# Optimization experiments

Measured on AMD Instinct MI355X. Metric: run time of the kernel, lower is better.

Reference implementation:

```python
import jax, jax.numpy as jnp
import numpy as np

IN_C, HID_C, OUT_C = 256, 512, 256
B, N = 8, 4096


def setup_inputs() -> dict:
    key = jax.random.key(0)
    ks = jax.random.split(key, 6)
    x = jax.random.normal(ks[0], (B, N, IN_C), dtype=jnp.float32)
    A = jax.random.uniform(ks[1], (B, N, N), dtype=jnp.float32)
    # Glorot-ish init for the two GCN layer weights + zero biases (PyG default bias=True)
    W1 = jax.random.normal(ks[2], (IN_C, HID_C), dtype=jnp.float32) * (1.0 / np.sqrt(IN_C))
    b1 = jnp.zeros((HID_C,), dtype=jnp.float32)
    W2 = jax.random.normal(ks[3], (HID_C, OUT_C), dtype=jnp.float32) * (1.0 / np.sqrt(HID_C))
    b2 = jnp.zeros((OUT_C,), dtype=jnp.float32)
    return {"x": x, "A": A, "W1": W1, "b1": b1, "W2": W2, "b2": b2}


def _gcn_norm(A):
    # dense equivalent of PyG gcn_norm with add_self_loops: A_hat = A + I,
    # norm = D^{-1/2} A_hat D^{-1/2}, with deg==0 -> 0 (inf guarded)
    A_hat = A + jnp.eye(A.shape[-1], dtype=A.dtype)  # [B,N,N]
    deg = A_hat.sum(axis=-1)                          # [B,N]
    d_inv_sqrt = jnp.where(deg > 0, jax.lax.rsqrt(jnp.maximum(deg, 1e-12)), 0.0)
    return d_inv_sqrt[:, :, None] * A_hat * d_inv_sqrt[:, None, :]


def reference(x, A, W1, b1, W2, b2):
    nrm = _gcn_norm(A)  # [B,N,N]
    # layer 1: out = A_hat_norm @ (x W1) + b1, then ReLU (dropout is identity in eval)
    h = jax.nn.relu(jnp.einsum('bij,bjh->bih', nrm, x @ W1) + b1)
    # layer 2
    out = jnp.einsum('bij,bjo->bio', nrm, h @ W2) + b2
    return out
```

## Files before the change

### kernel.cpp

```cpp
#include <hip/hip_runtime.h>
#include <stdint.h>

#define NN    4096
#define BATCH 8
#define IC    256
#define HC    512
#define OC    256
#define MTOT  (BATCH * NN)

typedef float    f32x4  __attribute__((ext_vector_type(4)));
typedef __bf16   bf16x8 __attribute__((ext_vector_type(8)));
typedef uint16_t u16x8  __attribute__((ext_vector_type(8)));
typedef uint16_t u16x4  __attribute__((ext_vector_type(4)));

__device__ __forceinline__ uint16_t f2b(float f) {
  union { float f; uint32_t u; } v; v.f = f;
  return (uint16_t)((v.u + 0x7FFFu + ((v.u >> 16) & 1u)) >> 16);
}

__device__ __forceinline__ void gl_lds16(const void* g, void* l) {
  __builtin_amdgcn_global_load_lds(
      (const __attribute__((address_space(1))) uint32_t*)g,
      (__attribute__((address_space(3))) uint32_t*)l, 16, 0, 0);
}

__global__ __launch_bounds__(512) void prep_kernel(const float* __restrict__ A,
                                                   uint16_t* __restrict__ Abf,
                                                   float* __restrict__ dinv) {
  const int bid = blockIdx.x;
  const int b = bid & 7, mt = bid >> 3;
  const int t = threadIdx.x;
  const int r = t >> 2, g = t & 3;
  const int rowl = mt * 128 + r;
  const float* Ap = A + ((size_t)b * NN + rowl) * NN + g * 8;
  uint16_t* Op = Abf + ((size_t)(b * 32 + mt) << 19) + r * 32 + ((g ^ (r & 3)) << 3);
  float s = 0.f;
  for (int kt = 0; kt < 128; ++kt) {
    f32x4 a0 = *(const f32x4*)(Ap + kt * 32);
    f32x4 a1 = *(const f32x4*)(Ap + kt * 32 + 4);
    int dj = rowl - (kt * 32 + g * 8);
    u16x8 o;
#pragma unroll
    for (int e = 0; e < 4; ++e) {
      float v0 = a0[e], v1 = a1[e];
      s += v0 + v1;
      if (dj == e)     v0 += 1.f;
      if (dj == e + 4) v1 += 1.f;
      o[e] = f2b(v0); o[e + 4] = f2b(v1);
    }
    *(u16x8*)(Op + (size_t)kt * 4096) = o;
  }
  __shared__ float red[512];
  red[t] = s;
  __syncthreads();
  if (t < 128) {
    float deg = red[t * 4] + red[t * 4 + 1] + red[t * 4 + 2] + red[t * 4 + 3] + 1.0f;
    dinv[b * NN + mt * 128 + t] = 1.0f / sqrtf(deg);
  }
}

template<bool ABF16, int KTOT, int NC>
__global__ __launch_bounds__(256, 2) void xw_kernel(const void* __restrict__ Av,
                                                    const float* __restrict__ W,
                                                    const float* __restrict__ dinv,
                                                    uint16_t* __restrict__ Vt) {
  constexpr int LDT = 72;
  __shared__ uint16_t smem[18432];
  uint16_t* as_ = smem;
  uint16_t* wt_ = smem + 9216;
  const int t = threadIdx.x;
  const int m0 = blockIdx.x * 128;
  const int n0 = blockIdx.y * 128;
  const int lane = t & 63, wid = t >> 6;
  const int wm = wid >> 1, wn = wid & 1;
  f32x4 acc[4][4] = {};

  for (int kt = 0; kt < KTOT / 64; ++kt) {
    const int k0 = kt * 64;
    __syncthreads();
    if constexpr (!ABF16) {
      const float* Ap = (const float*)Av;
      const int c4 = t & 15, r0 = t >> 4;
#pragma unroll
      for (int i = 0; i < 8; ++i) {
        int r = r0 + 16 * i;
        f32x4 v = *(const f32x4*)(Ap + (size_t)(m0 + r) * KTOT + k0 + c4 * 4);
        uint32_t lo = f2b(v[0]) | ((uint32_t)f2b(v[1]) << 16);
        uint32_t hi = f2b(v[2]) | ((uint32_t)f2b(v[3]) << 16);
        *(uint2*)&as_[r * LDT + c4 * 4] = make_uint2(lo, hi);
      }
    } else {
      const uint16_t* Ap = (const uint16_t*)Av;
      const int c8 = t & 7, r0 = t >> 3;
#pragma unroll
      for (int i = 0; i < 4; ++i) {
        int r = r0 + 32 * i;
        u16x8 v = *(const u16x8*)(Ap + (size_t)(m0 + r) * KTOT + k0 + c8 * 8);
        *(u16x8*)&as_[r * LDT + c8 * 8] = v;
      }
    }
    {
      const int n4 = t & 31, kq = t >> 5;
#pragma unroll
      for (int i = 0; i < 8; ++i) {
        int k = kq + 8 * i;
        f32x4 v = *(const f32x4*)(W + (size_t)(k0 + k) * NC + n0 + n4 * 4);
        uint16_t hv[4] = { f2b(v[0]), f2b(v[1]), f2b(v[2]), f2b(v[3]) };
#pragma unroll
        for (int w = 0; w < 4; ++w) {
          int we = (w + n4) & 3;
          wt_[(n4 * 4 + we) * LDT + k] = hv[we];
        }
      }
    }
    __syncthreads();
#pragma unroll
    for (int kk = 0; kk < 2; ++kk) {
      bf16x8 bfr[4], afr[4];
#pragma unroll
      for (int fn = 0; fn < 4; ++fn)
        bfr[fn] = *(const bf16x8*)&wt_[(wn * 64 + fn * 16 + (lane & 15)) * LDT + kk * 32 + (lane >> 4) * 8];
#pragma unroll
      for (int fm = 0; fm < 4; ++fm)
        afr[fm] = *(const bf16x8*)&as_[(wm * 64 + fm * 16 + (lane & 15)) * LDT + kk * 32 + (lane >> 4) * 8];
#pragma unroll
      for (int fm = 0; fm < 4; ++fm)
#pragma unroll
        for (int fn = 0; fn < 4; ++fn)
          acc[fm][fn] = __builtin_amdgcn_mfma_f32_16x16x32_bf16(afr[fm], bfr[fn], acc[fm][fn], 0, 0, 0);
    }
  }
  const int b = m0 >> 12;
  const int klocal = m0 & 4095;
  __syncthreads();
  uint16_t* lv = smem;
#pragma unroll
  for (int fm = 0; fm < 4; ++fm)
#pragma unroll
    for (int fn = 0; fn < 4; ++fn) {
      int nloc = wn * 64 + fn * 16 + (lane & 15);
      int ml0  = wm * 64 + fm * 16 + (lane >> 4) * 4;
      u16x4 pk;
#pragma unroll
      for (int r = 0; r < 4; ++r)
        pk[r] = f2b(acc[fm][fn][r] * dinv[m0 + ml0 + r]);
      *(u16x4*)&lv[nloc * 144 + ml0] = pk;
    }
  __syncthreads();
#pragma unroll
  for (int i = 0; i < 8; ++i) {
    int nloc = (t >> 4) + 16 * i;
    int ch = t & 15;
    u16x8 v = *(const u16x8*)&lv[nloc * 144 + ch * 8];
    int nglob = n0 + nloc;
    int ktv = (klocal >> 5) + (ch >> 2);
    int s = (ch & 3) ^ (nglob & 3);
    *(u16x8*)(Vt + (((size_t)b * 128 + ktv) * NC + nglob) * 32 + s * 8) = v;
  }
}

template<int NC_, bool RELU>
__global__ __launch_bounds__(512, 2) void agg_kernel(const uint16_t* __restrict__ Abf,
                                                     const uint16_t* __restrict__ Vt,
                                                     const float* __restrict__ dinv,
                                                     const float* __restrict__ bias,
                                                     uint16_t* __restrict__ Hout,
                                                     float* __restrict__ Fout) {
  constexpr int FN  = NC_ / 64;
  constexpr int WNE = NC_ / 4;
  constexpr int VPW = NC_ / 128;
  __shared__ uint16_t as_[2][4096];
  __shared__ uint16_t vt_[2][NC_ * 32];

  const int t = threadIdx.x;
  const int lane = t & 63, wid = t >> 6;
  const int wm = wid >> 2, wn = wid & 3;
  const int fr = lane & 15, c = lane >> 4;
  const int bid = blockIdx.x;
  const int b = bid & 7, mt = bid >> 3;

  const uint16_t* Abase = Abf + ((size_t)(b * 32 + mt) << 19);
  const uint16_t* Vbase = Vt + (size_t)b * NC_ * 4096;

  auto stage = [&](int kt, int buf) {
    const uint16_t* At = Abase + (size_t)kt * 4096;
    const uint16_t* Vtile = Vbase + (size_t)kt * (NC_ * 32);
    gl_lds16(At + wid * 512 + lane * 8, &as_[buf][wid * 512]);
#pragma unroll
    for (int i = 0; i < VPW; ++i) {
      int cv = wid * VPW + i;
      gl_lds16(Vtile + cv * 512 + lane * 8, &vt_[buf][cv * 512]);
    }
  };

  f32x4 acc[4][FN] = {};

  stage(0, 0);
  asm volatile("s_waitcnt vmcnt(0)" ::: "memory");
  asm volatile("" ::: "memory");
  __builtin_amdgcn_s_barrier();
  __builtin_amdgcn_sched_barrier(0);

  for (int kt = 0; kt < 128; ++kt) {
    const int cur = kt & 1;
    if (kt < 127) stage(kt + 1, cur ^ 1);
    bf16x8 afr[4], bfr[FN];
#pragma unroll
    for (int fm = 0; fm < 4; ++fm) {
      int row = wm * 64 + fm * 16 + fr;
      afr[fm] = *(const bf16x8*)&as_[cur][row * 32 + ((c ^ (row & 3)) << 3)];
    }
#pragma unroll
    for (int fn = 0; fn < FN; ++fn) {
      int n = wn * WNE + fn * 16 + fr;
      bfr[fn] = *(const bf16x8*)&vt_[cur][n * 32 + ((c ^ (n & 3)) << 3)];
    }
    __builtin_amdgcn_s_setprio(1);
#pragma unroll
    for (int fm = 0; fm < 4; ++fm)
#pragma unroll
      for (int fn = 0; fn < FN; ++fn)
        acc[fm][fn] = __builtin_amdgcn_mfma_f32_16x16x32_bf16(afr[fm], bfr[fn], acc[fm][fn], 0, 0, 0);
    __builtin_amdgcn_s_setprio(0);
    if (kt < 127) {
      asm volatile("s_waitcnt vmcnt(0)" ::: "memory");
      asm volatile("" ::: "memory");
      __builtin_amdgcn_s_barrier();
      __builtin_amdgcn_sched_barrier(0);
    }
  }
#pragma unroll
  for (int fm = 0; fm < 4; ++fm)
#pragma unroll
    for (int r = 0; r < 4; ++r) {
      size_t grow = (size_t)b * NN + mt * 128 + wm * 64 + fm * 16 + (lane >> 4) * 4 + r;
      float dv = dinv[grow];
#pragma unroll
      for (int fn = 0; fn < FN; ++fn) {
        int col = wn * WNE + fn * 16 + fr;
        float v = acc[fm][fn][r] * dv + bias[col];
        if constexpr (RELU) {
          Hout[grow * NC_ + col] = f2b(fmaxf(v, 0.f));
        } else {
          Fout[grow * NC_ + col] = v;
        }
      }
    }
}

extern "C" void kernel_launch(void* const* d_in, const int* in_sizes, int n_in,
                              void* d_out, int out_size, void* d_ws, size_t ws_size,
                              hipStream_t stream) {
  const float* x  = (const float*)d_in[0];
  const float* A  = (const float*)d_in[1];
  const float* W1 = (const float*)d_in[2];
  const float* b1 = (const float*)d_in[3];
  const float* W2 = (const float*)d_in[4];
  const float* b2 = (const float*)d_in[5];
  float* out = (float*)d_out;

  char* ws = (char*)d_ws;
  uint16_t* Abf  = (uint16_t*)ws;
  float*    dinv = (float*)(ws + 268435456);
  uint16_t* Vt   = (uint16_t*)(ws + 268435456 + 131072);
  uint16_t* H    = (uint16_t*)(ws + 268435456 + 131072 + 33554432);

  prep_kernel<<<256, 512, 0, stream>>>(A, Abf, dinv);
  xw_kernel<false, IC, HC><<<dim3(256, 4), 256, 0, stream>>>(x, W1, dinv, Vt);
  agg_kernel<HC, true><<<256, 512, 0, stream>>>(Abf, Vt, dinv, b1, H, nullptr);
  xw_kernel<true, HC, OC><<<dim3(256, 2), 256, 0, stream>>>(H, W2, dinv, Vt);
  agg_kernel<OC, false><<<256, 512, 0, stream>>>(Abf, Vt, dinv, b2, nullptr, out);
}
```

Measured before the change: 1.234 ms.

## Retile aggregation kernel to 64-row blocks with 4 waves and deeper K chunks

The aggregation kernel moves from 128-row tiles with 8 waves (2x4) to 64-row tiles with 4 waves, launching 512 blocks of 256 threads instead of 256 of 512. The second layer also stages two 32-wide K chunks per pipeline step, halving the number of barriers. The smaller M tile gives more blocks for the 256 CUs, but each V tile is now loaded twice as often across blocks, which raises global and L2 traffic for the aggregation.

```diff
diff --git a/kernel.cpp b/kernel.cpp
--- a/kernel.cpp
+++ b/kernel.cpp
@@ -6,7 +6,6 @@
 #define IC    256
 #define HC    512
 #define OC    256
-#define MTOT  (BATCH * NN)
 
 typedef float    f32x4  __attribute__((ext_vector_type(4)));
 typedef __bf16   bf16x8 __attribute__((ext_vector_type(8)));
@@ -159,37 +158,41 @@
   }
 }
 
-template<int NC_, bool RELU>
-__global__ __launch_bounds__(512, 2) void agg_kernel(const uint16_t* __restrict__ Abf,
+template<int NC_, int BK_, bool RELU>
+__global__ __launch_bounds__(256, 2) void agg_kernel(const uint16_t* __restrict__ Abf,
                                                      const uint16_t* __restrict__ Vt,
                                                      const float* __restrict__ dinv,
                                                      const float* __restrict__ bias,
                                                      uint16_t* __restrict__ Hout,
                                                      float* __restrict__ Fout) {
+  constexpr int KCH = BK_ / 32;
   constexpr int FN  = NC_ / 64;
   constexpr int WNE = NC_ / 4;
-  constexpr int VPW = NC_ / 128;
-  __shared__ uint16_t as_[2][4096];
-  __shared__ uint16_t vt_[2][NC_ * 32];
+  constexpr int VIW = NC_ / 64;
+  constexpr int NT  = 128 / KCH;
+  __shared__ uint16_t as_[2][KCH * 2048];
+  __shared__ uint16_t vt_[2][KCH * NC_ * 32];
 
   const int t = threadIdx.x;
   const int lane = t & 63, wid = t >> 6;
-  const int wm = wid >> 2, wn = wid & 3;
   const int fr = lane & 15, c = lane >> 4;
   const int bid = blockIdx.x;
-  const int b = bid & 7, mt = bid >> 3;
-
-  const uint16_t* Abase = Abf + ((size_t)(b * 32 + mt) << 19);
+  const int b = bid & 7, mtb = bid >> 3;
+
+  const uint16_t* Abase = Abf + (((size_t)(b * 32 + (mtb >> 1))) << 19) + (mtb & 1) * 2048;
   const uint16_t* Vbase = Vt + (size_t)b * NC_ * 4096;
 
   auto stage = [&](int kt, int buf) {
-    const uint16_t* At = Abase + (size_t)kt * 4096;
-    const uint16_t* Vtile = Vbase + (size_t)kt * (NC_ * 32);
-    gl_lds16(At + wid * 512 + lane * 8, &as_[buf][wid * 512]);
-#pragma unroll
-    for (int i = 0; i < VPW; ++i) {
-      int cv = wid * VPW + i;
-      gl_lds16(Vtile + cv * 512 + lane * 8, &vt_[buf][cv * 512]);
+#pragma unroll
+    for (int ch = 0; ch < KCH; ++ch) {
+      const uint16_t* At = Abase + (size_t)(kt * KCH + ch) * 4096;
+      gl_lds16(At + wid * 512 + lane * 8, &as_[buf][ch * 2048 + wid * 512]);
+      const uint16_t* Vtile = Vbase + (size_t)(kt * KCH + ch) * (NC_ * 32);
+#pragma unroll
+      for (int i = 0; i < VIW; ++i) {
+        int cv = wid * VIW + i;
+        gl_lds16(Vtile + cv * 512 + lane * 8, &vt_[buf][ch * NC_ * 32 + cv * 512]);
+      }
     }
   };
 
@@ -197,34 +200,35 @@
 
   stage(0, 0);
   asm volatile("s_waitcnt vmcnt(0)" ::: "memory");
-  asm volatile("" ::: "memory");
   __builtin_amdgcn_s_barrier();
   __builtin_amdgcn_sched_barrier(0);
 
-  for (int kt = 0; kt < 128; ++kt) {
+  for (int kt = 0; kt < NT; ++kt) {
     const int cur = kt & 1;
-    if (kt < 127) stage(kt + 1, cur ^ 1);
-    bf16x8 afr[4], bfr[FN];
-#pragma unroll
-    for (int fm = 0; fm < 4; ++fm) {
-      int row = wm * 64 + fm * 16 + fr;
-      afr[fm] = *(const bf16x8*)&as_[cur][row * 32 + ((c ^ (row & 3)) << 3)];
-    }
-#pragma unroll
-    for (int fn = 0; fn < FN; ++fn) {
-      int n = wn * WNE + fn * 16 + fr;
-      bfr[fn] = *(const bf16x8*)&vt_[cur][n * 32 + ((c ^ (n & 3)) << 3)];
-    }
-    __builtin_amdgcn_s_setprio(1);
-#pragma unroll
-    for (int fm = 0; fm < 4; ++fm)
-#pragma unroll
-      for (int fn = 0; fn < FN; ++fn)
-        acc[fm][fn] = __builtin_amdgcn_mfma_f32_16x16x32_bf16(afr[fm], bfr[fn], acc[fm][fn], 0, 0, 0);
-    __builtin_amdgcn_s_setprio(0);
-    if (kt < 127) {
+    if (kt + 1 < NT) stage(kt + 1, cur ^ 1);
+#pragma unroll
+    for (int kk = 0; kk < KCH; ++kk) {
+      bf16x8 afr[4], bfr[FN];
+#pragma unroll
+      for (int fm = 0; fm < 4; ++fm) {
+        int row = fm * 16 + fr;
+        afr[fm] = *(const bf16x8*)&as_[cur][kk * 2048 + row * 32 + ((c ^ (fr & 3)) << 3)];
+      }
+#pragma unroll
+      for (int fn = 0; fn < FN; ++fn) {
+        int n = wid * WNE + fn * 16 + fr;
+        bfr[fn] = *(const bf16x8*)&vt_[cur][kk * NC_ * 32 + n * 32 + ((c ^ (fr & 3)) << 3)];
+      }
+      __builtin_amdgcn_s_setprio(1);
+#pragma unroll
+      for (int fm = 0; fm < 4; ++fm)
+#pragma unroll
+        for (int fn = 0; fn < FN; ++fn)
+          acc[fm][fn] = __builtin_amdgcn_mfma_f32_16x16x32_bf16(afr[fm], bfr[fn], acc[fm][fn], 0, 0, 0);
+      __builtin_amdgcn_s_setprio(0);
+    }
+    if (kt + 1 < NT) {
       asm volatile("s_waitcnt vmcnt(0)" ::: "memory");
-      asm volatile("" ::: "memory");
       __builtin_amdgcn_s_barrier();
       __builtin_amdgcn_sched_barrier(0);
     }
@@ -233,11 +237,11 @@
   for (int fm = 0; fm < 4; ++fm)
 #pragma unroll
     for (int r = 0; r < 4; ++r) {
-      size_t grow = (size_t)b * NN + mt * 128 + wm * 64 + fm * 16 + (lane >> 4) * 4 + r;
+      size_t grow = (size_t)b * NN + mtb * 64 + fm * 16 + (lane >> 4) * 4 + r;
       float dv = dinv[grow];
 #pragma unroll
       for (int fn = 0; fn < FN; ++fn) {
-        int col = wn * WNE + fn * 16 + fr;
+        int col = wid * WNE + fn * 16 + fr;
         float v = acc[fm][fn][r] * dv + bias[col];
         if constexpr (RELU) {
           Hout[grow * NC_ + col] = f2b(fmaxf(v, 0.f));
@@ -267,7 +271,7 @@
 
   prep_kernel<<<256, 512, 0, stream>>>(A, Abf, dinv);
   xw_kernel<false, IC, HC><<<dim3(256, 4), 256, 0, stream>>>(x, W1, dinv, Vt);
-  agg_kernel<HC, true><<<256, 512, 0, stream>>>(Abf, Vt, dinv, b1, H, nullptr);
+  agg_kernel<HC, 32, true><<<512, 256, 0, stream>>>(Abf, Vt, dinv, b1, H, nullptr);
   xw_kernel<true, HC, OC><<<dim3(256, 2), 256, 0, stream>>>(H, W2, dinv, Vt);
-  agg_kernel<OC, false><<<256, 512, 0, stream>>>(Abf, Vt, dinv, b2, nullptr, out);
-}
+  agg_kernel<OC, 64, false><<<512, 256, 0, stream>>>(Abf, Vt, dinv, b2, nullptr, out);
+}
```

Result: faster. 1.167 ms (-5.4%).
